# Optimization experiments

Measured on AMD Instinct MI355X. Metric: run time of the kernel, lower is better.

Reference implementation:

```python
import jax, jax.numpy as jnp
import numpy as np

B, L, S, H, E, D = 2, 2048, 2048, 16, 64, 64


def setup_inputs() -> dict:
    key = jax.random.key(0)
    ks = jax.random.split(key, 6)
    return {
        "q1": jax.random.normal(ks[0], (B, L, H, E), dtype=jnp.float32),
        "k1": jax.random.normal(ks[1], (B, S, H, E), dtype=jnp.float32),
        "v1": jax.random.normal(ks[2], (B, S, H, D), dtype=jnp.float32),
        "q2": jax.random.normal(ks[3], (B, L, H, E), dtype=jnp.float32),
        "k2": jax.random.normal(ks[4], (B, S, H, E), dtype=jnp.float32),
        "v2": jax.random.normal(ks[5], (B, S, H, D), dtype=jnp.float32),
        "attn_mask": 0,  # accepted but unused by the original forward
    }


def reference(q1, k1, v1, q2, k2, v2, attn_mask):
    # scale = 1/sqrt(E) (self.scale is None in init_kwargs)
    scale = 1.0 / jnp.sqrt(jnp.asarray(q1.shape[-1], dtype=q1.dtype))
    # dual QK scores: [B,H,L,S]
    scores1 = jnp.einsum('blhe,bshe->bhls', q1, k1)
    scores2 = jnp.einsum('blhe,bshe->bhls', q2, k2)
    # eval-mode (dropout disabled for deterministic reference)
    A = jnp.tanh(scores1 * scale) * jax.nn.sigmoid(scores2 * scale)
    # weighted V matmul: [B,L,H,D]
    out = jnp.einsum('bhls,bshd->blhd', A, v1)
    return out
```

## Files before the change

kernel.cpp:

```cpp
#include <hip/hip_runtime.h>

constexpr int Bc = 2, Lc = 2048, Sc = 2048, Hc = 16, Ec = 64, Dc = 64;
constexpr int TILES = Sc / 64;
constexpr int NBH   = Bc * Hc;
constexpr size_t TILE_ELEMS = 4096;
constexpr size_t ARR_ELEMS  = (size_t)NBH * TILES * TILE_ELEMS;
constexpr size_t WS_NEED    = ARR_ELEMS * 2 * 3;

typedef float          f32x4  __attribute__((ext_vector_type(4)));
typedef float          f32x16 __attribute__((ext_vector_type(16)));
typedef __bf16         bf16x8 __attribute__((ext_vector_type(8)));
typedef unsigned short u16x8  __attribute__((ext_vector_type(8)));
typedef unsigned short u16x4  __attribute__((ext_vector_type(4)));
typedef unsigned int   u32x4  __attribute__((ext_vector_type(4)));

static __device__ __forceinline__ unsigned cvtpk(float lo, float hi) {
    unsigned r;
    asm("v_cvt_pk_bf16_f32 %0, %1, %2" : "=v"(r) : "v"(lo), "v"(hi));
    return r;
}

static __device__ __forceinline__ void gl2lds16(const void* g, void* l) {
    __builtin_amdgcn_global_load_lds(
        (const __attribute__((address_space(1))) unsigned int*)g,
        (__attribute__((address_space(3))) unsigned int*)l, 16, 0, 0);
}

static __device__ __forceinline__ float fexp2(float x) {
#if __has_builtin(__builtin_amdgcn_exp2f)
    return __builtin_amdgcn_exp2f(x);
#else
    return exp2f(x);
#endif
}

__global__ __launch_bounds__(256) void prepass_kernel(
    const float* __restrict__ k1, const float* __restrict__ k2,
    const float* __restrict__ v1,
    unsigned short* __restrict__ k1b, unsigned short* __restrict__ k2b,
    unsigned short* __restrict__ vb)
{
    __shared__ unsigned short vt[64 * 80];

    const int blk = blockIdx.x;
    const int st  = blk & 31;
    const int bh  = blk >> 5;
    const int b   = bh >> 4, h = bh & 15;
    const int s0  = st * 64;
    const size_t tileo = (size_t)blk * TILE_ELEMS;

    #pragma unroll
    for (int it = 0; it < 2; ++it) {
        int u  = threadIdx.x + it * 256;
        int s  = u >> 3, e8 = u & 7;
        size_t g = ((size_t)((b * Sc + s0 + s) * Hc + h)) * Ec + e8 * 8;

        float4 x0 = *reinterpret_cast<const float4*>(k1 + g);
        float4 x1 = *reinterpret_cast<const float4*>(k1 + g + 4);
        u32x4 o;
        o[0] = cvtpk(x0.x, x0.y); o[1] = cvtpk(x0.z, x0.w);
        o[2] = cvtpk(x1.x, x1.y); o[3] = cvtpk(x1.z, x1.w);
        *reinterpret_cast<u32x4*>(&k1b[tileo + (size_t)(e8 * 64 + s) * 8]) = o;

        x0 = *reinterpret_cast<const float4*>(k2 + g);
        x1 = *reinterpret_cast<const float4*>(k2 + g + 4);
        o[0] = cvtpk(x0.x, x0.y); o[1] = cvtpk(x0.z, x0.w);
        o[2] = cvtpk(x1.x, x1.y); o[3] = cvtpk(x1.z, x1.w);
        *reinterpret_cast<u32x4*>(&k2b[tileo + (size_t)(e8 * 64 + s) * 8]) = o;

        x0 = *reinterpret_cast<const float4*>(v1 + g);
        x1 = *reinterpret_cast<const float4*>(v1 + g + 4);
        o[0] = cvtpk(x0.x, x0.y); o[1] = cvtpk(x0.z, x0.w);
        o[2] = cvtpk(x1.x, x1.y); o[3] = cvtpk(x1.z, x1.w);
        *reinterpret_cast<u32x4*>(&vt[s * 80 + e8 * 8]) = o;
    }
    __syncthreads();

    #pragma unroll
    for (int it = 0; it < 2; ++it) {
        int u  = threadIdx.x + it * 256;
        int d  = u >> 3, sc8 = u & 7;
        u16x8 o;
        #pragma unroll
        for (int j = 0; j < 8; ++j) o[j] = vt[(sc8 * 8 + j) * 80 + d];
        *reinterpret_cast<u16x8*>(&vb[tileo + (size_t)(sc8 * 64 + d) * 8]) = o;
    }
}

__global__ __launch_bounds__(256, 3) void fused_kernel(
    const float* __restrict__ q1, const float* __restrict__ q2,
    const unsigned short* __restrict__ k1b, const unsigned short* __restrict__ k2b,
    const unsigned short* __restrict__ vb, float* __restrict__ out)
{
    __shared__ unsigned short klds[2][2][4096];
    __shared__ unsigned short vlds[2][4096];

    const int orig    = blockIdx.x;
    const int logical = (orig & 7) * 128 + (orig >> 3);
    const int lblk = logical & 31;
    const int bh   = logical >> 5;
    const int b    = bh >> 4, h = bh & 15;

    const int tid  = threadIdx.x;
    const int w    = tid >> 6;
    const int lane = tid & 63;
    const int l31  = lane & 31;
    const int hi   = lane >> 5;
    const int qsub = w >> 1;
    const int sh   = w & 1;

    constexpr float C1 = 0.36067376022224085f;
    constexpr float C2 = -0.18033688011112043f;
    const int    qrow  = lblk * 64 + qsub * 32 + l31;
    const size_t qbase = ((size_t)((b * Lc + qrow) * Hc + h)) * Ec;
    u32x4 qa1[4], qa2[4];
    #pragma unroll
    for (int es = 0; es < 4; ++es) {
        const float* p1 = q1 + qbase + es * 16 + hi * 8;
        const float* p2 = q2 + qbase + es * 16 + hi * 8;
        float4 x0 = *reinterpret_cast<const float4*>(p1);
        float4 x1 = *reinterpret_cast<const float4*>(p1 + 4);
        qa1[es] = (u32x4){cvtpk(x0.x * C1, x0.y * C1), cvtpk(x0.z * C1, x0.w * C1),
                          cvtpk(x1.x * C1, x1.y * C1), cvtpk(x1.z * C1, x1.w * C1)};
        x0 = *reinterpret_cast<const float4*>(p2);
        x1 = *reinterpret_cast<const float4*>(p2 + 4);
        qa2[es] = (u32x4){cvtpk(x0.x * C2, x0.y * C2), cvtpk(x0.z * C2, x0.w * C2),
                          cvtpk(x1.x * C2, x1.y * C2), cvtpk(x1.z * C2, x1.w * C2)};
    }

    f32x16 acc0 = {}, acc1 = {};

    const unsigned short* k1g = k1b + (size_t)bh * TILES * TILE_ELEMS;
    const unsigned short* k2g = k2b + (size_t)bh * TILES * TILE_ELEMS;
    const unsigned short* vg  = vb  + (size_t)bh * TILES * TILE_ELEMS;

    const int srow = sh * 32 + l31;
    int koff[4];
    #pragma unroll
    for (int es = 0; es < 4; ++es)
        koff[es] = ((es * 2 + hi) * 64 + srow) * 8;

    int voff[4];
    #pragma unroll
    for (int dt = 0; dt < 2; ++dt)
        #pragma unroll
        for (int ks = 0; ks < 2; ++ks)
            voff[dt * 2 + ks] = ((sh * 4 + ks * 2 + hi) * 64 + dt * 32 + l31) * 8;

    {
        const size_t tb = (size_t)tid * 8;
        gl2lds16(k1g + tb,        &klds[0][0][tid * 8]);
        gl2lds16(k1g + tb + 2048, &klds[0][0][tid * 8 + 2048]);
        gl2lds16(k2g + tb,        &klds[0][1][tid * 8]);
        gl2lds16(k2g + tb + 2048, &klds[0][1][tid * 8 + 2048]);
        gl2lds16(vg  + tb,        &vlds[0][tid * 8]);
        gl2lds16(vg  + tb + 2048, &vlds[0][tid * 8 + 2048]);
    }

    int cur = 0;
    for (int st = 0; st < TILES; ++st) {
        __syncthreads();
        if (st + 1 < TILES) {
            const size_t tb = (size_t)(st + 1) * TILE_ELEMS + tid * 8;
            const int nxt = cur ^ 1;
            gl2lds16(k1g + tb,        &klds[nxt][0][tid * 8]);
            gl2lds16(k1g + tb + 2048, &klds[nxt][0][tid * 8 + 2048]);
            gl2lds16(k2g + tb,        &klds[nxt][1][tid * 8]);
            gl2lds16(k2g + tb + 2048, &klds[nxt][1][tid * 8 + 2048]);
            gl2lds16(vg  + tb,        &vlds[nxt][tid * 8]);
            gl2lds16(vg  + tb + 2048, &vlds[nxt][tid * 8 + 2048]);
        }

        const unsigned short* k1l = &klds[cur][0][0];
        const unsigned short* k2l = &klds[cur][1][0];
        f32x16 s1a = {}, s2a = {};
        #pragma unroll
        for (int es = 0; es < 4; ++es) {
            bf16x8 kf1 = __builtin_bit_cast(bf16x8, *reinterpret_cast<const u16x8*>(&k1l[koff[es]]));
            bf16x8 kf2 = __builtin_bit_cast(bf16x8, *reinterpret_cast<const u16x8*>(&k2l[koff[es]]));
            s1a = __builtin_amdgcn_mfma_f32_32x32x16_bf16(kf1, __builtin_bit_cast(bf16x8, qa1[es]), s1a, 0, 0, 0);
            s2a = __builtin_amdgcn_mfma_f32_32x32x16_bf16(kf2, __builtin_bit_cast(bf16x8, qa2[es]), s2a, 0, 0, 0);
        }

        const unsigned short* vl = &vlds[cur][0];
        u16x8 vfr[4];
        #pragma unroll
        for (int i = 0; i < 4; ++i)
            vfr[i] = *reinterpret_cast<const u16x8*>(&vl[voff[i]]);

        float p[16];
        #pragma unroll
        for (int i = 0; i < 16; ++i) {
            float t  = fexp2(s1a[i]);
            float uu = fexp2(s2a[i]);
            p[i] = (t - 1.f) * __builtin_amdgcn_rcpf((t + 1.f) * (1.f + uu));
        }

        #pragma unroll
        for (int ks = 0; ks < 2; ++ks) {
            unsigned A0 = cvtpk(p[8 * ks + 0], p[8 * ks + 1]);
            unsigned A1 = cvtpk(p[8 * ks + 2], p[8 * ks + 3]);
            unsigned B0 = cvtpk(p[8 * ks + 4], p[8 * ks + 5]);
            unsigned B1 = cvtpk(p[8 * ks + 6], p[8 * ks + 7]);
            asm("v_permlane32_swap_b32 %0, %1" : "+v"(A0), "+v"(B0));
            asm("v_permlane32_swap_b32 %0, %1" : "+v"(A1), "+v"(B1));
            bf16x8 pa = __builtin_bit_cast(bf16x8, (u32x4){A0, A1, B0, B1});
            acc0 = __builtin_amdgcn_mfma_f32_32x32x16_bf16(pa, __builtin_bit_cast(bf16x8, vfr[ks]),     acc0, 0, 0, 0);
            acc1 = __builtin_amdgcn_mfma_f32_32x32x16_bf16(pa, __builtin_bit_cast(bf16x8, vfr[2 + ks]), acc1, 0, 0, 0);
        }

        cur ^= 1;
    }

    __syncthreads();
    float* mbuf = reinterpret_cast<float*>(&klds[0][0][0]);
    if (sh == 1) {
        #pragma unroll
        for (int r4 = 0; r4 < 4; ++r4) {
            *reinterpret_cast<f32x4*>(&mbuf[(qsub * 2 + 0) * 1280 + lane * 20 + r4 * 4]) =
                (f32x4){acc0[r4 * 4 + 0], acc0[r4 * 4 + 1], acc0[r4 * 4 + 2], acc0[r4 * 4 + 3]};
            *reinterpret_cast<f32x4*>(&mbuf[(qsub * 2 + 1) * 1280 + lane * 20 + r4 * 4]) =
                (f32x4){acc1[r4 * 4 + 0], acc1[r4 * 4 + 1], acc1[r4 * 4 + 2], acc1[r4 * 4 + 3]};
        }
    }
    __syncthreads();
    if (sh == 0) {
        #pragma unroll
        for (int dt = 0; dt < 2; ++dt) {
            float m[16];
            #pragma unroll
            for (int r4 = 0; r4 < 4; ++r4) {
                f32x4 v = *reinterpret_cast<const f32x4*>(&mbuf[(qsub * 2 + dt) * 1280 + lane * 20 + r4 * 4]);
                m[r4 * 4 + 0] = v[0]; m[r4 * 4 + 1] = v[1]; m[r4 * 4 + 2] = v[2]; m[r4 * 4 + 3] = v[3];
            }
            #pragma unroll
            for (int r = 0; r < 16; ++r) {
                float val = m[r] + (dt == 0 ? acc0[r] : acc1[r]);
                int q = lblk * 64 + qsub * 32 + (r & 3) + 8 * (r >> 2) + 4 * hi;
                out[((size_t)(b * Lc + q) * Hc + h) * Dc + dt * 32 + l31] = val;
            }
        }
    }
}

static __device__ __forceinline__ unsigned short f2bf(float f) {
    unsigned u = __builtin_bit_cast(unsigned, f);
    u += 0x7fffu + ((u >> 16) & 1u);
    return (unsigned short)(u >> 16);
}

__global__ __launch_bounds__(256) void fallback_kernel(
    const float* __restrict__ q1, const float* __restrict__ k1,
    const float* __restrict__ v1, const float* __restrict__ q2,
    const float* __restrict__ k2, float* __restrict__ out)
{
    constexpr int KSTR = 72, VSTR = 88, PSTR = 88;
    __shared__ unsigned short k1t[64 * KSTR];
    __shared__ unsigned short k2t[64 * KSTR];
    __shared__ unsigned short vtt[64 * VSTR];
    __shared__ unsigned short pt [4 * 16 * PSTR];

    const int blk  = blockIdx.x;
    const int lblk = blk & 31;
    const int bh   = blk >> 5;
    const int b    = bh >> 4;
    const int h    = bh & 15;
    const int tid  = threadIdx.x;
    const int w    = tid >> 6;
    const int lane = tid & 63;
    const int lr   = lane & 15;
    const int lg   = lane >> 4;

    const int    qrow  = lblk * 64 + w * 16 + lr;
    const size_t qbase = ((size_t)(b * Lc + qrow) * Hc + h) * Ec;
    bf16x8 a1[2], a2[2];
    for (int es = 0; es < 2; ++es) {
        u16x8 t1, t2;
        for (int j = 0; j < 8; ++j) {
            t1[j] = f2bf(q1[qbase + es * 32 + lg * 8 + j]);
            t2[j] = f2bf(q2[qbase + es * 32 + lg * 8 + j]);
        }
        a1[es] = __builtin_bit_cast(bf16x8, t1);
        a2[es] = __builtin_bit_cast(bf16x8, t2);
    }
    f32x4 acc[4];
    for (int i = 0; i < 4; ++i) acc[i] = (f32x4){0.f, 0.f, 0.f, 0.f};
    constexpr float CT = 0.25f, CS = -0.125f;

    for (int s0 = 0; s0 < Sc; s0 += 64) {
        for (int it = 0; it < 4; ++it) {
            int idx = tid + it * 256;
            int sr  = idx >> 4;
            int c4  = (idx & 15) << 2;
            size_t gk = ((size_t)(b * Sc + s0 + sr) * Hc + h) * Ec + c4;
            float4 x1 = *reinterpret_cast<const float4*>(k1 + gk);
            float4 x2 = *reinterpret_cast<const float4*>(k2 + gk);
            float4 xv = *reinterpret_cast<const float4*>(v1 + gk);
            u16x4 o1, o2;
            o1[0]=f2bf(x1.x); o1[1]=f2bf(x1.y); o1[2]=f2bf(x1.z); o1[3]=f2bf(x1.w);
            o2[0]=f2bf(x2.x); o2[1]=f2bf(x2.y); o2[2]=f2bf(x2.z); o2[3]=f2bf(x2.w);
            *reinterpret_cast<u16x4*>(&k1t[sr * KSTR + c4]) = o1;
            *reinterpret_cast<u16x4*>(&k2t[sr * KSTR + c4]) = o2;
            vtt[(c4 + 0) * VSTR + sr] = f2bf(xv.x);
            vtt[(c4 + 1) * VSTR + sr] = f2bf(xv.y);
            vtt[(c4 + 2) * VSTR + sr] = f2bf(xv.z);
            vtt[(c4 + 3) * VSTR + sr] = f2bf(xv.w);
        }
        __syncthreads();
        for (int ct = 0; ct < 4; ++ct) {
            f32x4 s1 = {0.f,0.f,0.f,0.f}, s2 = {0.f,0.f,0.f,0.f};
            for (int es = 0; es < 2; ++es) {
                bf16x8 b1 = __builtin_bit_cast(bf16x8,
                    *reinterpret_cast<const u16x8*>(&k1t[(ct*16 + lr) * KSTR + es*32 + lg*8]));
                bf16x8 b2 = __builtin_bit_cast(bf16x8,
                    *reinterpret_cast<const u16x8*>(&k2t[(ct*16 + lr) * KSTR + es*32 + lg*8]));
                s1 = __builtin_amdgcn_mfma_f32_16x16x32_bf16(a1[es], b1, s1, 0, 0, 0);
                s2 = __builtin_amdgcn_mfma_f32_16x16x32_bf16(a2[es], b2, s2, 0, 0, 0);
            }
            for (int i = 0; i < 4; ++i) {
                float xa = fminf(fmaxf(s1[i] * CT, -30.f), 30.f);
                float xb = fminf(fmaxf(s2[i] * CS, -30.f), 30.f);
                float t  = __expf(xa);
                float u  = __expf(xb);
                float p  = (t - 1.f) * __builtin_amdgcn_rcpf((t + 1.f) * (1.f + u));
                pt[(w*16 + lg*4 + i) * PSTR + ct*16 + lr] = f2bf(p);
            }
        }
        asm volatile("s_waitcnt lgkmcnt(0)" ::: "memory");
        for (int ks = 0; ks < 2; ++ks) {
            bf16x8 pa = __builtin_bit_cast(bf16x8,
                *reinterpret_cast<const u16x8*>(&pt[(w*16 + lr) * PSTR + ks*32 + lg*8]));
            for (int dt = 0; dt < 4; ++dt) {
                bf16x8 vf = __builtin_bit_cast(bf16x8,
                    *reinterpret_cast<const u16x8*>(&vtt[(dt*16 + lr) * VSTR + ks*32 + lg*8]));
                acc[dt] = __builtin_amdgcn_mfma_f32_16x16x32_bf16(pa, vf, acc[dt], 0, 0, 0);
            }
        }
        __syncthreads();
    }
    const int orow = lblk * 64 + w * 16;
    for (int dt = 0; dt < 4; ++dt)
        for (int i = 0; i < 4; ++i) {
            int l = orow + lg * 4 + i;
            out[((size_t)(b * Lc + l) * Hc + h) * Dc + dt * 16 + lr] = acc[dt][i];
        }
}

extern "C" void kernel_launch(void* const* d_in, const int* in_sizes, int n_in,
                              void* d_out, int out_size, void* d_ws, size_t ws_size,
                              hipStream_t stream) {
    const float* q1 = (const float*)d_in[0];
    const float* k1 = (const float*)d_in[1];
    const float* v1 = (const float*)d_in[2];
    const float* q2 = (const float*)d_in[3];
    const float* k2 = (const float*)d_in[4];
    float* out = (float*)d_out;

    if (ws_size >= WS_NEED) {
        unsigned short* k1b = (unsigned short*)d_ws;
        unsigned short* k2b = k1b + ARR_ELEMS;
        unsigned short* vbp = k2b + ARR_ELEMS;
        prepass_kernel<<<dim3(NBH * TILES), dim3(256), 0, stream>>>(k1, k2, v1, k1b, k2b, vbp);
        fused_kernel<<<dim3(NBH * TILES), dim3(256), 0, stream>>>(q1, q2, k1b, k2b, vbp, out);
    } else {
        fallback_kernel<<<dim3(NBH * TILES), dim3(256), 0, stream>>>(q1, k1, v1, q2, k2, out);
    }
}
```

Before: 114.8 us.

## Load K/V fragments directly from global memory, dropping LDS double buffering

Replaces the LDS double-buffered staging of K1/K2/V tiles (global_load_lds plus a barrier per tile) with direct per-lane vector loads from global memory into registers, relying on L2/cache reuse across waves. This removes the per-iteration __syncthreads and frees the shared memory, keeping only the reduction buffer, which may allow higher occupancy. The exp2 helper is also switched to the OCML native exp2. The trade-off is that each wave now fetches K/V independently, with no explicit prefetch to overlap load latency with MFMA work, so more global traffic and exposed latency are possible.

```diff
diff --git a/kernel.cpp b/kernel.cpp
--- a/kernel.cpp
+++ b/kernel.cpp
@@ -14,24 +14,16 @@
 typedef unsigned short u16x4  __attribute__((ext_vector_type(4)));
 typedef unsigned int   u32x4  __attribute__((ext_vector_type(4)));
 
+extern "C" __device__ float __ocml_native_exp2_f32(float);
+
 static __device__ __forceinline__ unsigned cvtpk(float lo, float hi) {
     unsigned r;
     asm("v_cvt_pk_bf16_f32 %0, %1, %2" : "=v"(r) : "v"(lo), "v"(hi));
     return r;
 }
 
-static __device__ __forceinline__ void gl2lds16(const void* g, void* l) {
-    __builtin_amdgcn_global_load_lds(
-        (const __attribute__((address_space(1))) unsigned int*)g,
-        (__attribute__((address_space(3))) unsigned int*)l, 16, 0, 0);
-}
-
 static __device__ __forceinline__ float fexp2(float x) {
-#if __has_builtin(__builtin_amdgcn_exp2f)
-    return __builtin_amdgcn_exp2f(x);
-#else
-    return exp2f(x);
-#endif
+    return __ocml_native_exp2_f32(x);
 }
 
 __global__ __launch_bounds__(256) void prepass_kernel(
@@ -92,8 +84,7 @@
     const unsigned short* __restrict__ k1b, const unsigned short* __restrict__ k2b,
     const unsigned short* __restrict__ vb, float* __restrict__ out)
 {
-    __shared__ unsigned short klds[2][2][4096];
-    __shared__ unsigned short vlds[2][4096];
+    __shared__ float mbuf[4 * 1280];
 
     const int orig    = blockIdx.x;
     const int logical = (orig & 7) * 128 + (orig >> 3);
@@ -147,46 +138,30 @@
         for (int ks = 0; ks < 2; ++ks)
             voff[dt * 2 + ks] = ((sh * 4 + ks * 2 + hi) * 64 + dt * 32 + l31) * 8;
 
-    {
-        const size_t tb = (size_t)tid * 8;
-        gl2lds16(k1g + tb,        &klds[0][0][tid * 8]);
-        gl2lds16(k1g + tb + 2048, &klds[0][0][tid * 8 + 2048]);
-        gl2lds16(k2g + tb,        &klds[0][1][tid * 8]);
-        gl2lds16(k2g + tb + 2048, &klds[0][1][tid * 8 + 2048]);
-        gl2lds16(vg  + tb,        &vlds[0][tid * 8]);
-        gl2lds16(vg  + tb + 2048, &vlds[0][tid * 8 + 2048]);
-    }
-
-    int cur = 0;
     for (int st = 0; st < TILES; ++st) {
-        __syncthreads();
-        if (st + 1 < TILES) {
-            const size_t tb = (size_t)(st + 1) * TILE_ELEMS + tid * 8;
-            const int nxt = cur ^ 1;
-            gl2lds16(k1g + tb,        &klds[nxt][0][tid * 8]);
-            gl2lds16(k1g + tb + 2048, &klds[nxt][0][tid * 8 + 2048]);
-            gl2lds16(k2g + tb,        &klds[nxt][1][tid * 8]);
-            gl2lds16(k2g + tb + 2048, &klds[nxt][1][tid * 8 + 2048]);
-            gl2lds16(vg  + tb,        &vlds[nxt][tid * 8]);
-            gl2lds16(vg  + tb + 2048, &vlds[nxt][tid * 8 + 2048]);
-        }
-
-        const unsigned short* k1l = &klds[cur][0][0];
-        const unsigned short* k2l = &klds[cur][1][0];
+        const unsigned short* kt1 = k1g + (size_t)st * TILE_ELEMS;
+        const unsigned short* kt2 = k2g + (size_t)st * TILE_ELEMS;
+        const unsigned short* vt  = vg  + (size_t)st * TILE_ELEMS;
+
+        u16x8 kf1[4], kf2[4];
+        #pragma unroll
+        for (int es = 0; es < 4; ++es) {
+            kf1[es] = *reinterpret_cast<const u16x8*>(&kt1[koff[es]]);
+            kf2[es] = *reinterpret_cast<const u16x8*>(&kt2[koff[es]]);
+        }
+        u16x8 vfr[4];
+        #pragma unroll
+        for (int i = 0; i < 4; ++i)
+            vfr[i] = *reinterpret_cast<const u16x8*>(&vt[voff[i]]);
+
         f32x16 s1a = {}, s2a = {};
         #pragma unroll
         for (int es = 0; es < 4; ++es) {
-            bf16x8 kf1 = __builtin_bit_cast(bf16x8, *reinterpret_cast<const u16x8*>(&k1l[koff[es]]));
-            bf16x8 kf2 = __builtin_bit_cast(bf16x8, *reinterpret_cast<const u16x8*>(&k2l[koff[es]]));
-            s1a = __builtin_amdgcn_mfma_f32_32x32x16_bf16(kf1, __builtin_bit_cast(bf16x8, qa1[es]), s1a, 0, 0, 0);
-            s2a = __builtin_amdgcn_mfma_f32_32x32x16_bf16(kf2, __builtin_bit_cast(bf16x8, qa2[es]), s2a, 0, 0, 0);
-        }
-
-        const unsigned short* vl = &vlds[cur][0];
-        u16x8 vfr[4];
-        #pragma unroll
-        for (int i = 0; i < 4; ++i)
-            vfr[i] = *reinterpret_cast<const u16x8*>(&vl[voff[i]]);
+            s1a = __builtin_amdgcn_mfma_f32_32x32x16_bf16(
+                __builtin_bit_cast(bf16x8, kf1[es]), __builtin_bit_cast(bf16x8, qa1[es]), s1a, 0, 0, 0);
+            s2a = __builtin_amdgcn_mfma_f32_32x32x16_bf16(
+                __builtin_bit_cast(bf16x8, kf2[es]), __builtin_bit_cast(bf16x8, qa2[es]), s2a, 0, 0, 0);
+        }
 
         float p[16];
         #pragma unroll
@@ -208,12 +183,9 @@
             acc0 = __builtin_amdgcn_mfma_f32_32x32x16_bf16(pa, __builtin_bit_cast(bf16x8, vfr[ks]),     acc0, 0, 0, 0);
             acc1 = __builtin_amdgcn_mfma_f32_32x32x16_bf16(pa, __builtin_bit_cast(bf16x8, vfr[2 + ks]), acc1, 0, 0, 0);
         }
-
-        cur ^= 1;
     }
 
     __syncthreads();
-    float* mbuf = reinterpret_cast<float*>(&klds[0][0][0]);
     if (sh == 1) {
         #pragma unroll
         for (int r4 = 0; r4 < 4; ++r4) {
```

Result: no change. 116.4 us (+1.5%).
